# Optimization experiments

Hardware: AMD Instinct MI355X
Metric: run time of the kernel (lower is better)

Reference implementation:

```python
import jax, jax.numpy as jnp
import numpy as np

EMBED = 1024
HEADS = 16
HEAD_DIM = EMBED // HEADS
B, S = 2, 2048


def setup_inputs() -> dict:
    key = jax.random.key(0)
    ks = jax.random.split(key, 9)
    std = 1.0 / np.sqrt(EMBED)
    def lin(k):
        kw, kb = jax.random.split(k)
        W = jax.random.uniform(kw, (EMBED, EMBED), jnp.float32, -std, std)
        b = jax.random.uniform(kb, (EMBED,), jnp.float32, -std, std)
        return W, b
    Wq, bq = lin(ks[0])
    Wk, bk = lin(ks[1])
    Wv, bv = lin(ks[2])
    Wo, bo = lin(ks[3])
    x = jax.random.normal(ks[4], (B, S, EMBED), jnp.float32)
    return {"x": x, "Wq": Wq, "bq": bq, "Wk": Wk, "bk": bk,
            "Wv": Wv, "bv": bv, "Wo": Wo, "bo": bo}


def reference(x, Wq, bq, Wk, bk, Wv, bv, Wo, bo):
    b, s, e = x.shape
    # projections (torch Linear: x @ W^T + b; here W stored as [in,out])
    Q = x @ Wq + bq
    K = x @ Wk + bk
    V = x @ Wv + bv
    # [b, h, s, d]
    Q = Q.reshape(b, s, HEADS, HEAD_DIM).transpose(0, 2, 1, 3)
    K = K.reshape(b, s, HEADS, HEAD_DIM).transpose(0, 2, 1, 3)
    V = V.reshape(b, s, HEADS, HEAD_DIM).transpose(0, 2, 1, 3)
    scores = jnp.einsum('bhqd,bhkd->bhqk', Q, K) / np.sqrt(HEAD_DIM)
    # causal mask: positions k > q masked to -inf
    causal = jnp.tril(jnp.ones((s, s), dtype=bool))
    scores = jnp.where(causal[None, None], scores, -jnp.inf)
    weights = jax.nn.softmax(scores, axis=-1)
    out = jnp.einsum('bhqk,bhkd->bhqd', weights, V)
    out = out.transpose(0, 2, 1, 3).reshape(b, s, e)
    return out @ Wo + bo
```

## Files before the change

kernel.cpp:

```cpp
#include <hip/hip_runtime.h>
#include <hip/hip_bf16.h>
#include <stdint.h>

#define EMBED 1024
#define HEADS 16
#define HDIM 64
#define BATCH 2
#define SEQ 2048
#define NROWS (BATCH*SEQ)

typedef __attribute__((ext_vector_type(8))) short short8;
typedef __attribute__((ext_vector_type(4))) float f32x4;

#define LOG2E 1.44269504088896f

__device__ __forceinline__ unsigned short f2bf(float f) {
    __hip_bfloat16 b = __float2bfloat16(f);
    return *reinterpret_cast<unsigned short*>(&b);
}

__device__ __forceinline__ unsigned cvt_pk_bf16(float lo, float hi) {
    unsigned r;
    asm("v_cvt_pk_bf16_f32 %0, %1, %2" : "=v"(r) : "v"(lo), "v"(hi));
    return r;
}

__device__ __forceinline__ short8 mk8(unsigned a, unsigned b, unsigned c, unsigned d) {
    union { unsigned u[4]; short8 s; } x;
    x.u[0] = a; x.u[1] = b; x.u[2] = c; x.u[3] = d;
    return x.s;
}

__device__ __forceinline__ void g2l16(const void* g, void* l) {
    __builtin_amdgcn_global_load_lds(
        (const __attribute__((address_space(1))) unsigned int*)g,
        (__attribute__((address_space(3))) unsigned int*)l, 16, 0, 0);
}

__global__ void cast_x_kernel(const float* __restrict__ x,
                              unsigned short* __restrict__ xb, int n4) {
    int i = blockIdx.x * blockDim.x + threadIdx.x;
    if (i < n4) {
        float4 v = reinterpret_cast<const float4*>(x)[i];
        ushort4 o;
        o.x = f2bf(v.x); o.y = f2bf(v.y); o.z = f2bf(v.z); o.w = f2bf(v.w);
        reinterpret_cast<ushort4*>(xb)[i] = o;
    }
}

__global__ void transW4_kernel(const float* __restrict__ W0,
                               const float* __restrict__ W1,
                               const float* __restrict__ W2,
                               const float* __restrict__ W3,
                               unsigned short* __restrict__ dst) {
    __shared__ float tile[32][33];
    const int z = blockIdx.z;
    const float* W = (z == 0) ? W0 : (z == 1) ? W1 : (z == 2) ? W2 : W3;
    unsigned short* Wt = dst + (size_t)z * EMBED * EMBED;
    int tx = threadIdx.x, ty = threadIdx.y;
#pragma unroll
    for (int r = 0; r < 4; r++) {
        int i = blockIdx.y * 32 + ty + r * 8;
        int o = blockIdx.x * 32 + tx;
        tile[ty + r * 8][tx] = W[(size_t)i * EMBED + o];
    }
    __syncthreads();
    int i2 = blockIdx.y * 32 + tx;
#pragma unroll
    for (int r = 0; r < 4; r++) {
        int o2 = blockIdx.x * 32 + ty + r * 8;
        Wt[(size_t)o2 * EMBED + i2] = f2bf(tile[tx][ty + r * 8]);
    }
}

template<int MODE, int BM>
__global__ __launch_bounds__(256)
void gemm_kernel(const unsigned short* __restrict__ A,
                 const unsigned short* __restrict__ B,
                 int K,
                 unsigned short* __restrict__ Qo,
                 unsigned short* __restrict__ Ko,
                 unsigned short* __restrict__ Vto,
                 const float* __restrict__ bq,
                 const float* __restrict__ bk,
                 const float* __restrict__ bvv,
                 float* __restrict__ Co,
                 const float* __restrict__ bo) {
    constexpr int AI = BM / 32;
    __shared__ __attribute__((aligned(16))) unsigned short As[BM * 64];
    __shared__ __attribute__((aligned(16))) unsigned short Bs[128 * 64];
    const int t = threadIdx.x;
    const int lane = t & 63;
    const int w = t >> 6;
    const int wr = w >> 1, wc = w & 1;
    const int l15 = lane & 15, l16 = lane >> 4;

    int bx, by;
    {
        const int xcd = blockIdx.x & 7;
        const int r = blockIdx.x >> 3;
        if (MODE == 0) {
            bx = (xcd & 1) * 12 + r % 12;
            by = (xcd >> 1) * 8 + r / 12;
        } else {
            bx = r & 7;
            by = xcd * 8 + (r >> 3);
        }
    }
    const int m0 = by * BM;
    const int n0 = bx * 128;

    f32x4 acc[AI][4];
#pragma unroll
    for (int i = 0; i < AI; i++)
#pragma unroll
        for (int j = 0; j < 4; j++) acc[i][j] = (f32x4){0.f, 0.f, 0.f, 0.f};

    for (int k0 = 0; k0 < K; k0 += 64) {
        __syncthreads();
#pragma unroll
        for (int i = 0; i < BM / 32; i++) {
            int c = i * 256 + t;
            int row = c >> 3;
            int lc = (c & 7) ^ (row & 7);
            g2l16(A + (size_t)(m0 + row) * K + k0 + lc * 8,
                  As + (size_t)(i * 256 + (t & ~63)) * 8);
        }
#pragma unroll
        for (int i = 0; i < 4; i++) {
            int c = i * 256 + t;
            int row = c >> 3;
            int lc = (c & 7) ^ (row & 7);
            g2l16(B + (size_t)(n0 + row) * K + k0 + lc * 8,
                  Bs + (size_t)(i * 256 + (t & ~63)) * 8);
        }
        __syncthreads();
#pragma unroll
        for (int kk = 0; kk < 2; kk++) {
            short8 a[AI], b[4];
#pragma unroll
            for (int ai = 0; ai < AI; ai++) {
                int row = wr * (BM / 2) + ai * 16 + l15;
                int ch = kk * 4 + l16;
                a[ai] = *reinterpret_cast<const short8*>(
                    As + row * 64 + ((ch ^ (row & 7)) << 3));
            }
#pragma unroll
            for (int bj = 0; bj < 4; bj++) {
                int row = wc * 64 + bj * 16 + l15;
                int ch = kk * 4 + l16;
                b[bj] = *reinterpret_cast<const short8*>(
                    Bs + row * 64 + ((ch ^ (row & 7)) << 3));
            }
            __builtin_amdgcn_s_setprio(1);
#pragma unroll
            for (int ai = 0; ai < AI; ai++)
#pragma unroll
                for (int bj = 0; bj < 4; bj++)
                    acc[ai][bj] = __builtin_amdgcn_mfma_f32_16x16x32_bf16(
                        a[ai], b[bj], acc[ai][bj], 0, 0, 0);
            __builtin_amdgcn_s_setprio(0);
        }
    }

    if (MODE == 0) {
        const int which = n0 >> 10;
        const int coln = n0 & 1023;
        const float* bias = which == 0 ? bq : (which == 1 ? bk : bvv);
        const float scale = which == 0 ? 0.125f * LOG2E : 1.0f;
#pragma unroll
        for (int ai = 0; ai < AI; ai++) {
            int rowb = m0 + wr * (BM / 2) + ai * 16 + l16 * 4;
            int b_ = rowb >> 11;
            int s = rowb & 2047;
#pragma unroll
            for (int bj = 0; bj < 4; bj++) {
                int col = coln + wc * 64 + bj * 16 + l15;
                float bsv = bias[col];
                int h = col >> 6, d = col & 63;
                if (which < 2) {
                    unsigned short* dst = (which == 0) ? Qo : Ko;
                    size_t base = ((size_t)(b_ * HEADS + h)) * SEQ * HDIM;
#pragma unroll
                    for (int r = 0; r < 4; r++) {
                        float v = (acc[ai][bj][r] + bsv) * scale;
                        dst[base + (size_t)(s + r) * HDIM + d] = f2bf(v);
                    }
                } else {
                    ushort4 pk;
                    pk.x = f2bf(acc[ai][bj][0] + bsv);
                    pk.y = f2bf(acc[ai][bj][1] + bsv);
                    pk.z = f2bf(acc[ai][bj][2] + bsv);
                    pk.w = f2bf(acc[ai][bj][3] + bsv);
                    int cs = (s >> 2) & 15;
                    int ps = (cs & 8) | ((cs & 3) << 1) | ((cs >> 2) & 1);
                    size_t off = ((size_t)(b_ * HEADS + h) * HDIM + d) * SEQ +
                                 (size_t)((s & ~63) | (ps << 2));
                    *reinterpret_cast<ushort4*>(Vto + off) = pk;
                }
            }
        }
    } else {
#pragma unroll
        for (int ai = 0; ai < AI; ai++) {
            int rowb = m0 + wr * (BM / 2) + ai * 16 + l16 * 4;
#pragma unroll
            for (int bj = 0; bj < 4; bj++) {
                int col = n0 + wc * 64 + bj * 16 + l15;
                float bsv = bo[col];
#pragma unroll
                for (int r = 0; r < 4; r++)
                    Co[(size_t)(rowb + r) * EMBED + col] = acc[ai][bj][r] + bsv;
            }
        }
    }
}

__device__ __forceinline__ void stage_kv(const unsigned short* __restrict__ Kg,
                                         const unsigned short* __restrict__ Vg,
                                         int kv0, unsigned short* Ksb,
                                         unsigned short* Vsb, int tl) {
#pragma unroll
    for (int i = 0; i < 4; i++) {
        int c = i * 128 + tl;
        int row = c >> 3;
        int lc = (c & 7) ^ (row & 7);
        g2l16(Kg + (size_t)(kv0 + row) * HDIM + lc * 8,
              Ksb + (i * 128 + (tl & ~63)) * 8);
    }
#pragma unroll
    for (int i = 0; i < 4; i++) {
        int c = i * 128 + tl;
        int d = c >> 3;
        int lc = (c & 7) ^ (d & 7);
        g2l16(Vg + (size_t)d * SEQ + kv0 + lc * 8,
              Vsb + (i * 128 + (tl & ~63)) * 8);
    }
}

__global__ __launch_bounds__(256, 2)
void attn_kernel(const unsigned short* __restrict__ Q,
                 const unsigned short* __restrict__ Kk,
                 const unsigned short* __restrict__ Vt,
                 unsigned short* __restrict__ O) {
    __shared__ __attribute__((aligned(16))) unsigned short Ks[4][64 * 64];
    __shared__ __attribute__((aligned(16))) unsigned short Vs[4][64 * 64];

    const int t = threadIdx.x;
    const int lane = t & 63;
    const int w = t >> 6;
    const int wq = w >> 1;
    const int wk = w & 1;
    const int l15 = lane & 15, l16 = lane >> 4;

    const int id = blockIdx.x;
    const int xcd = id & 7;
    const int u = id >> 3;
    const int bh = xcd * 4 + (u & 3);
    const int su = u >> 2;
    const int qi = (su < 16) ? su : 47 - su;
    const int q0 = qi * 64;
    const size_t base = (size_t)bh * SEQ * HDIM;
    const unsigned short* Kg = Kk + base;
    const unsigned short* Vg = Vt + base;
    const int qrow0 = q0 + wq * 32;

    short8 qf[2][2];
    {
        const unsigned short* Qg = Q + base + (size_t)qrow0 * HDIM;
#pragma unroll
        for (int qb = 0; qb < 2; qb++)
#pragma unroll
            for (int kc = 0; kc < 2; kc++)
                qf[qb][kc] = *reinterpret_cast<const short8*>(
                    Qg + (qb * 16 + l15) * HDIM + (kc * 4 + l16) * 8);
    }

    f32x4 oacc[2][4];
#pragma unroll
    for (int qb = 0; qb < 2; qb++)
#pragma unroll
        for (int nd = 0; nd < 4; nd++) oacc[qb][nd] = (f32x4){0.f, 0.f, 0.f, 0.f};
    float m_run[2] = {-1e30f, -1e30f};
    float l_run[2] = {0.f, 0.f};

    const int nt = qi + 1;
    const int nsuper = (nt + 1) >> 1;

    auto stagepair = [&](int ta, int tb) {
        if (t < 128) {
            if (ta < nt) stage_kv(Kg, Vg, ta * 64, Ks[ta & 3], Vs[ta & 3], t);
        } else {
            if (tb < nt) stage_kv(Kg, Vg, tb * 64, Ks[tb & 3], Vs[tb & 3], t - 128);
        }
    };

    auto qkt = [&](f32x4 (&sc)[2][4], const unsigned short* Kb) {
#pragma unroll
        for (int qb = 0; qb < 2; qb++)
#pragma unroll
            for (int kb = 0; kb < 4; kb++) sc[qb][kb] = (f32x4){0.f, 0.f, 0.f, 0.f};
#pragma unroll
        for (int kc = 0; kc < 2; kc++) {
            short8 ka[4];
#pragma unroll
            for (int kb = 0; kb < 4; kb++) {
                int row = kb * 16 + l15;
                ka[kb] = *reinterpret_cast<const short8*>(
                    Kb + row * 64 + (((kc * 4 + l16) ^ (row & 7)) << 3));
            }
            __builtin_amdgcn_s_setprio(1);
#pragma unroll
            for (int qb = 0; qb < 2; qb++)
#pragma unroll
                for (int kb = 0; kb < 4; kb++)
                    sc[qb][kb] = __builtin_amdgcn_mfma_f32_16x16x32_bf16(
                        ka[kb], qf[qb][kc], sc[qb][kb], 0, 0, 0);
            __builtin_amdgcn_s_setprio(0);
        }
    };

    auto softmax_pv = [&](f32x4 (&sc)[2][4], const unsigned short* Vb, bool diag) {
        if (diag) {
#pragma unroll
            for (int qb = 0; qb < 2; qb++) {
                const int qloc = wq * 32 + qb * 16 + l15;
#pragma unroll
                for (int kb = 0; kb < 4; kb++)
#pragma unroll
                    for (int r = 0; r < 4; r++) {
                        int kloc = kb * 16 + l16 * 4 + r;
                        sc[qb][kb][r] = (kloc > qloc) ? -1e30f : sc[qb][kb][r];
                    }
            }
        }
        float vmax[2];
        bool need = false;
#pragma unroll
        for (int qb = 0; qb < 2; qb++) {
            float mx = -1e30f;
#pragma unroll
            for (int kb = 0; kb < 4; kb++)
                mx = fmaxf(mx, fmaxf(fmaxf(sc[qb][kb][0], sc[qb][kb][1]),
                                     fmaxf(sc[qb][kb][2], sc[qb][kb][3])));
            vmax[qb] = mx;
            need = need || (mx > m_run[qb] + 8.0f);
        }
        if (__any(need)) {
#pragma unroll
            for (int qb = 0; qb < 2; qb++) {
                float mx = vmax[qb];
                mx = fmaxf(mx, __shfl_xor(mx, 16));
                mx = fmaxf(mx, __shfl_xor(mx, 32));
                float mn = fmaxf(m_run[qb], mx);
                float sf = __builtin_amdgcn_exp2f(m_run[qb] - mn);
                m_run[qb] = mn;
                l_run[qb] *= sf;
#pragma unroll
                for (int r = 0; r < 4; r++) {
                    float sfr = __shfl(sf, l16 * 4 + r);
#pragma unroll
                    for (int nd = 0; nd < 4; nd++) oacc[qb][nd][r] *= sfr;
                }
            }
        }
        short8 pa[2][2];
#pragma unroll
        for (int qb = 0; qb < 2; qb++) {
            float p[4][4];
            float ps = 0.f;
#pragma unroll
            for (int kb = 0; kb < 4; kb++)
#pragma unroll
                for (int r = 0; r < 4; r++) {
                    p[kb][r] = __builtin_amdgcn_exp2f(sc[qb][kb][r] - m_run[qb]);
                    ps += p[kb][r];
                }
            pa[qb][0] = mk8(cvt_pk_bf16(p[0][0], p[0][1]),
                            cvt_pk_bf16(p[0][2], p[0][3]),
                            cvt_pk_bf16(p[1][0], p[1][1]),
                            cvt_pk_bf16(p[1][2], p[1][3]));
            pa[qb][1] = mk8(cvt_pk_bf16(p[2][0], p[2][1]),
                            cvt_pk_bf16(p[2][2], p[2][3]),
                            cvt_pk_bf16(p[3][0], p[3][1]),
                            cvt_pk_bf16(p[3][2], p[3][3]));
            l_run[qb] += ps;
        }
#pragma unroll
        for (int m = 0; m < 2; m++) {
            short8 vb[4];
#pragma unroll
            for (int nd = 0; nd < 4; nd++) {
                int row = nd * 16 + l15;
                vb[nd] = *reinterpret_cast<const short8*>(
                    Vb + row * 64 + (((m * 4 + l16) ^ (row & 7)) << 3));
            }
            __builtin_amdgcn_s_setprio(1);
#pragma unroll
            for (int qb = 0; qb < 2; qb++)
#pragma unroll
                for (int nd = 0; nd < 4; nd++)
                    oacc[qb][nd] = __builtin_amdgcn_mfma_f32_16x16x32_bf16(
                        pa[qb][m], vb[nd], oacc[qb][nd], 0, 0, 0);
            __builtin_amdgcn_s_setprio(0);
        }
    };

    f32x4 sc[2][4];

    stagepair(0, 1);
    asm volatile("s_waitcnt vmcnt(0)" ::: "memory");
    __builtin_amdgcn_s_barrier();
    asm volatile("" ::: "memory");
    stagepair(2, 3);
    int myt = wk;
    if (myt < nt) qkt(sc, Ks[myt & 3]);

    for (int j = 1; j < nsuper; j++) {
        if (myt < nt) softmax_pv(sc, Vs[myt & 3], false);
        asm volatile("s_waitcnt vmcnt(0)" ::: "memory");
        __builtin_amdgcn_s_barrier();
        asm volatile("" ::: "memory");
        stagepair(2 * j + 2, 2 * j + 3);
        int tc = 2 * j + wk;
        if (tc < nt) qkt(sc, Ks[tc & 3]);
        myt = tc;
    }
    if (myt < nt) softmax_pv(sc, Vs[myt & 3], myt == nt - 1);

    __syncthreads();
    float* po = reinterpret_cast<float*>(&Ks[0][0]);
    float* pml = reinterpret_cast<float*>(&Vs[0][0]);
    if (wk == 1) {
#pragma unroll
        for (int qb = 0; qb < 2; qb++) {
#pragma unroll
            for (int nd = 0; nd < 4; nd++)
                reinterpret_cast<f32x4*>(po)[(((wq << 1) | qb) * 4 + nd) * 64 + lane] =
                    oacc[qb][nd];
            pml[((((wq << 1) | qb) * 64) + lane) * 2]     = m_run[qb];
            pml[((((wq << 1) | qb) * 64) + lane) * 2 + 1] = l_run[qb];
        }
    }
    __syncthreads();
    if (wk == 0) {
        const int b_ = bh >> 4, h = bh & 15;
#pragma unroll
        for (int qb = 0; qb < 2; qb++) {
            float m1 = pml[((((wq << 1) | qb) * 64) + lane) * 2];
            float l1 = pml[((((wq << 1) | qb) * 64) + lane) * 2 + 1];
            float ms = fmaxf(m_run[qb], m1);
            float a0 = __builtin_amdgcn_exp2f(m_run[qb] - ms);
            float a1 = __builtin_amdgcn_exp2f(m1 - ms);
            float lmp = l_run[qb] * a0 + l1 * a1;
            lmp += __shfl_xor(lmp, 16);
            lmp += __shfl_xor(lmp, 32);
            f32x4 o1[4];
#pragma unroll
            for (int nd = 0; nd < 4; nd++)
                o1[nd] = reinterpret_cast<f32x4*>(po)[(((wq << 1) | qb) * 4 + nd) * 64 + lane];
            float li = 1.0f / lmp;
#pragma unroll
            for (int r = 0; r < 4; r++) {
                float a0r = __shfl(a0, l16 * 4 + r);
                float a1r = __shfl(a1, l16 * 4 + r);
                float lir = __shfl(li, l16 * 4 + r);
                int row = b_ * SEQ + qrow0 + qb * 16 + l16 * 4 + r;
#pragma unroll
                for (int nd = 0; nd < 4; nd++) {
                    float v = oacc[qb][nd][r] * a0r + o1[nd][r] * a1r;
                    O[(size_t)row * EMBED + h * 64 + nd * 16 + l15] = f2bf(v * lir);
                }
            }
        }
    }
}

extern "C" void kernel_launch(void* const* d_in, const int* in_sizes, int n_in,
                              void* d_out, int out_size, void* d_ws, size_t ws_size,
                              hipStream_t stream) {
    (void)in_sizes; (void)n_in; (void)out_size; (void)ws_size;
    const float* x  = (const float*)d_in[0];
    const float* Wq = (const float*)d_in[1];
    const float* bq = (const float*)d_in[2];
    const float* Wk = (const float*)d_in[3];
    const float* bk = (const float*)d_in[4];
    const float* Wv = (const float*)d_in[5];
    const float* bv = (const float*)d_in[6];
    const float* Wo = (const float*)d_in[7];
    const float* bo = (const float*)d_in[8];
    float* out = (float*)d_out;

    unsigned short* xb   = (unsigned short*)d_ws;
    unsigned short* Wqkv = xb + (size_t)NROWS * EMBED;
    unsigned short* Wot  = Wqkv + (size_t)3 * EMBED * EMBED;
    unsigned short* Qb   = Wot + (size_t)EMBED * EMBED;
    unsigned short* Kb   = Qb + (size_t)NROWS * EMBED;
    unsigned short* Vtb  = Kb + (size_t)NROWS * EMBED;
    unsigned short* attn = Vtb + (size_t)NROWS * EMBED;

    cast_x_kernel<<<(NROWS * EMBED / 4 + 255) / 256, 256, 0, stream>>>(
        x, xb, NROWS * EMBED / 4);
    transW4_kernel<<<dim3(32, 32, 4), dim3(32, 8), 0, stream>>>(
        Wq, Wk, Wv, Wo, Wqkv);

    gemm_kernel<0, 128><<<768, 256, 0, stream>>>(
        xb, Wqkv, EMBED, Qb, Kb, Vtb, bq, bk, bv, nullptr, nullptr);

    attn_kernel<<<1024, 256, 0, stream>>>(Qb, Kb, Vtb, attn);

    gemm_kernel<1, 64><<<512, 256, 0, stream>>>(
        attn, Wot, EMBED, nullptr, nullptr, nullptr, nullptr, nullptr, nullptr,
        out, bo);
}
```

Before: 94.84 us.

## Merge prep kernels and double-buffer output projection GEMM with smaller tiles

The x cast and the four weight transposes now run in one prep kernel, which saves a launch. The output-projection GEMM now uses 64x64 tiles, so the grid doubles to 1024 blocks and more CUs get work. It also gains a double-buffered LDS pipeline that issues the next K-tile load before computing the current one. In exchange, each block reuses less data per tile, and the new per-iteration vmcnt(0) wait plus barrier may limit how much of the load is actually hidden.

```diff
diff --git a/kernel.cpp b/kernel.cpp
--- a/kernel.cpp
+++ b/kernel.cpp
@@ -37,10 +37,38 @@
         (__attribute__((address_space(3))) unsigned int*)l, 16, 0, 0);
 }
 
-__global__ void cast_x_kernel(const float* __restrict__ x,
-                              unsigned short* __restrict__ xb, int n4) {
-    int i = blockIdx.x * blockDim.x + threadIdx.x;
-    if (i < n4) {
+__global__ void prep_kernel(const float* __restrict__ x,
+                            unsigned short* __restrict__ xb,
+                            const float* __restrict__ W0,
+                            const float* __restrict__ W1,
+                            const float* __restrict__ W2,
+                            const float* __restrict__ W3,
+                            unsigned short* __restrict__ dst) {
+    __shared__ float tile[32][33];
+    const int id = blockIdx.x;
+    const int t = threadIdx.x;
+    if (id < 4096) {
+        const int z = id >> 10;
+        const int by = (id >> 5) & 31;
+        const int bx = id & 31;
+        const float* W = (z == 0) ? W0 : (z == 1) ? W1 : (z == 2) ? W2 : W3;
+        unsigned short* Wt = dst + (size_t)z * EMBED * EMBED;
+        const int tx = t & 31, ty = t >> 5;
+#pragma unroll
+        for (int r = 0; r < 4; r++) {
+            int i = by * 32 + ty + r * 8;
+            int o = bx * 32 + tx;
+            tile[ty + r * 8][tx] = W[(size_t)i * EMBED + o];
+        }
+        __syncthreads();
+        int i2 = by * 32 + tx;
+#pragma unroll
+        for (int r = 0; r < 4; r++) {
+            int o2 = bx * 32 + ty + r * 8;
+            Wt[(size_t)o2 * EMBED + i2] = f2bf(tile[tx][ty + r * 8]);
+        }
+    } else {
+        int i = (id - 4096) * 256 + t;
         float4 v = reinterpret_cast<const float4*>(x)[i];
         ushort4 o;
         o.x = f2bf(v.x); o.y = f2bf(v.y); o.z = f2bf(v.z); o.w = f2bf(v.w);
@@ -48,32 +76,7 @@
     }
 }
 
-__global__ void transW4_kernel(const float* __restrict__ W0,
-                               const float* __restrict__ W1,
-                               const float* __restrict__ W2,
-                               const float* __restrict__ W3,
-                               unsigned short* __restrict__ dst) {
-    __shared__ float tile[32][33];
-    const int z = blockIdx.z;
-    const float* W = (z == 0) ? W0 : (z == 1) ? W1 : (z == 2) ? W2 : W3;
-    unsigned short* Wt = dst + (size_t)z * EMBED * EMBED;
-    int tx = threadIdx.x, ty = threadIdx.y;
-#pragma unroll
-    for (int r = 0; r < 4; r++) {
-        int i = blockIdx.y * 32 + ty + r * 8;
-        int o = blockIdx.x * 32 + tx;
-        tile[ty + r * 8][tx] = W[(size_t)i * EMBED + o];
-    }
-    __syncthreads();
-    int i2 = blockIdx.y * 32 + tx;
-#pragma unroll
-    for (int r = 0; r < 4; r++) {
-        int o2 = blockIdx.x * 32 + ty + r * 8;
-        Wt[(size_t)o2 * EMBED + i2] = f2bf(tile[tx][ty + r * 8]);
-    }
-}
-
-template<int MODE, int BM>
+template<int MODE, int BM, int BN, int PIPE>
 __global__ __launch_bounds__(256)
 void gemm_kernel(const unsigned short* __restrict__ A,
                  const unsigned short* __restrict__ B,
@@ -87,8 +90,10 @@
                  float* __restrict__ Co,
                  const float* __restrict__ bo) {
     constexpr int AI = BM / 32;
-    __shared__ __attribute__((aligned(16))) unsigned short As[BM * 64];
-    __shared__ __attribute__((aligned(16))) unsigned short Bs[128 * 64];
+    constexpr int BJ = BN / 32;
+    constexpr int NBUF = PIPE ? 2 : 1;
+    __shared__ __attribute__((aligned(16))) unsigned short As[NBUF][BM * 64];
+    __shared__ __attribute__((aligned(16))) unsigned short Bs[NBUF][BN * 64];
     const int t = threadIdx.x;
     const int lane = t & 63;
     const int w = t >> 6;
@@ -103,63 +108,86 @@
             bx = (xcd & 1) * 12 + r % 12;
             by = (xcd >> 1) * 8 + r / 12;
         } else {
-            bx = r & 7;
-            by = xcd * 8 + (r >> 3);
+            bx = r & 15;
+            by = xcd * 8 + (r >> 4);
         }
     }
     const int m0 = by * BM;
-    const int n0 = bx * 128;
-
-    f32x4 acc[AI][4];
+    const int n0 = bx * BN;
+
+    f32x4 acc[AI][BJ];
 #pragma unroll
     for (int i = 0; i < AI; i++)
 #pragma unroll
-        for (int j = 0; j < 4; j++) acc[i][j] = (f32x4){0.f, 0.f, 0.f, 0.f};
-
-    for (int k0 = 0; k0 < K; k0 += 64) {
-        __syncthreads();
+        for (int j = 0; j < BJ; j++) acc[i][j] = (f32x4){0.f, 0.f, 0.f, 0.f};
+
+    auto stage = [&](int k0, int buf) {
 #pragma unroll
         for (int i = 0; i < BM / 32; i++) {
             int c = i * 256 + t;
             int row = c >> 3;
             int lc = (c & 7) ^ (row & 7);
             g2l16(A + (size_t)(m0 + row) * K + k0 + lc * 8,
-                  As + (size_t)(i * 256 + (t & ~63)) * 8);
-        }
-#pragma unroll
-        for (int i = 0; i < 4; i++) {
+                  As[buf] + (size_t)(i * 256 + (t & ~63)) * 8);
+        }
+#pragma unroll
+        for (int i = 0; i < BN / 32; i++) {
             int c = i * 256 + t;
             int row = c >> 3;
             int lc = (c & 7) ^ (row & 7);
             g2l16(B + (size_t)(n0 + row) * K + k0 + lc * 8,
-                  Bs + (size_t)(i * 256 + (t & ~63)) * 8);
-        }
-        __syncthreads();
+                  Bs[buf] + (size_t)(i * 256 + (t & ~63)) * 8);
+        }
+    };
+
+    auto compute = [&](int buf) {
 #pragma unroll
         for (int kk = 0; kk < 2; kk++) {
-            short8 a[AI], b[4];
+            short8 a[AI], b[BJ];
 #pragma unroll
             for (int ai = 0; ai < AI; ai++) {
                 int row = wr * (BM / 2) + ai * 16 + l15;
                 int ch = kk * 4 + l16;
                 a[ai] = *reinterpret_cast<const short8*>(
-                    As + row * 64 + ((ch ^ (row & 7)) << 3));
-            }
-#pragma unroll
-            for (int bj = 0; bj < 4; bj++) {
-                int row = wc * 64 + bj * 16 + l15;
+                    As[buf] + row * 64 + ((ch ^ (row & 7)) << 3));
+            }
+#pragma unroll
+            for (int bj = 0; bj < BJ; bj++) {
+                int row = wc * (BN / 2) + bj * 16 + l15;
                 int ch = kk * 4 + l16;
                 b[bj] = *reinterpret_cast<const short8*>(
-                    Bs + row * 64 + ((ch ^ (row & 7)) << 3));
+                    Bs[buf] + row * 64 + ((ch ^ (row & 7)) << 3));
             }
             __builtin_amdgcn_s_setprio(1);
 #pragma unroll
             for (int ai = 0; ai < AI; ai++)
 #pragma unroll
-                for (int bj = 0; bj < 4; bj++)
+                for (int bj = 0; bj < BJ; bj++)
                     acc[ai][bj] = __builtin_amdgcn_mfma_f32_16x16x32_bf16(
                         a[ai], b[bj], acc[ai][bj], 0, 0, 0);
             __builtin_amdgcn_s_setprio(0);
+        }
+    };
+
+    if (PIPE) {
+        const int ntk = K >> 6;
+        stage(0, 0);
+        asm volatile("s_waitcnt vmcnt(0)" ::: "memory");
+        __builtin_amdgcn_s_barrier();
+        asm volatile("" ::: "memory");
+        for (int tk = 0; tk < ntk; tk++) {
+            if (tk + 1 < ntk) stage((tk + 1) << 6, (tk + 1) & 1);
+            compute(tk & 1);
+            asm volatile("s_waitcnt vmcnt(0)" ::: "memory");
+            __builtin_amdgcn_s_barrier();
+            asm volatile("" ::: "memory");
+        }
+    } else {
+        for (int k0 = 0; k0 < K; k0 += 64) {
+            __syncthreads();
+            stage(k0, 0);
+            __syncthreads();
+            compute(0);
         }
     }
 
@@ -174,8 +202,8 @@
             int b_ = rowb >> 11;
             int s = rowb & 2047;
 #pragma unroll
-            for (int bj = 0; bj < 4; bj++) {
-                int col = coln + wc * 64 + bj * 16 + l15;
+            for (int bj = 0; bj < BJ; bj++) {
+                int col = coln + wc * (BN / 2) + bj * 16 + l15;
                 float bsv = bias[col];
                 int h = col >> 6, d = col & 63;
                 if (which < 2) {
@@ -205,8 +233,8 @@
         for (int ai = 0; ai < AI; ai++) {
             int rowb = m0 + wr * (BM / 2) + ai * 16 + l16 * 4;
 #pragma unroll
-            for (int bj = 0; bj < 4; bj++) {
-                int col = n0 + wc * 64 + bj * 16 + l15;
+            for (int bj = 0; bj < BJ; bj++) {
+                int col = n0 + wc * (BN / 2) + bj * 16 + l15;
                 float bsv = bo[col];
 #pragma unroll
                 for (int r = 0; r < 4; r++)
@@ -499,17 +527,14 @@
     unsigned short* Vtb  = Kb + (size_t)NROWS * EMBED;
     unsigned short* attn = Vtb + (size_t)NROWS * EMBED;
 
-    cast_x_kernel<<<(NROWS * EMBED / 4 + 255) / 256, 256, 0, stream>>>(
-        x, xb, NROWS * EMBED / 4);
-    transW4_kernel<<<dim3(32, 32, 4), dim3(32, 8), 0, stream>>>(
-        Wq, Wk, Wv, Wo, Wqkv);
-
-    gemm_kernel<0, 128><<<768, 256, 0, stream>>>(
+    prep_kernel<<<8192, 256, 0, stream>>>(x, xb, Wq, Wk, Wv, Wo, Wqkv);
+
+    gemm_kernel<0, 128, 128, 0><<<768, 256, 0, stream>>>(
         xb, Wqkv, EMBED, Qb, Kb, Vtb, bq, bk, bv, nullptr, nullptr);
 
     attn_kernel<<<1024, 256, 0, stream>>>(Qb, Kb, Vtb, attn);
 
-    gemm_kernel<1, 64><<<512, 256, 0, stream>>>(
+    gemm_kernel<1, 64, 64, 1><<<1024, 256, 0, stream>>>(
         attn, Wot, EMBED, nullptr, nullptr, nullptr, nullptr, nullptr, nullptr,
         out, bo);
 }
```

New measurement: 91.07 us. -4.0%, faster.
